# Kernel optimization log

Measured on AMD Instinct MI355X. Metric: run time of the kernel, lower is better.

The kernel has to match this reference:

```python
import jax, jax.numpy as jnp
import numpy as np

B, TQ, TKV, NPR, H, D = 4, 1024, 1024, 5, 16, 64
IN, OUT, R, P, NT = 1024, H * D, 64, 4096, 4
KV = NPR + TKV  # prompt tokens prepended to kv sequence


def setup_inputs() -> dict:
    key = jax.random.key(0)
    ks = jax.random.split(key, 20)
    n = lambda k, shp, s: jax.random.normal(k, shp, jnp.float32) * s
    W = 0.02  # weight init scale
    return {
        "pe": n(ks[0], (P, OUT), 1.0),
        "attn_output": n(ks[1], (B, TQ, OUT), 1.0),
        "q": n(ks[2], (B, H, TQ, D), 1.0),
        "kv_query": n(ks[3], (B, TKV, IN), 1.0),
        "attn_mask": jnp.zeros((TQ, KV), jnp.float32),
        "prompt": n(ks[4], (NT, NPR, IN), 1.0),
        "gates": n(ks[5], (1,), 1.0),
        "k_w1": n(ks[6], (IN, R), W), "k_w2": n(ks[7], (R, OUT), W),
        "v_w1": n(ks[8], (IN, R), W), "v_w2": n(ks[9], (R, OUT), W),
        "kp_w1": n(ks[10], (OUT, R), W), "kp_w2": n(ks[11], (R, OUT), W),
        "qp_w1": n(ks[12], (OUT, R), W), "qp_w2": n(ks[13], (R, OUT), W),
        "indices_a": jax.random.randint(ks[14], (B, TQ), 0, P),
        "indices_b": jax.random.randint(ks[15], (B, TKV), 0, P),
        "task_idx": jax.random.randint(ks[16], (B,), 0, NT),
    }


def reference(pe, attn_output, q, kv_query, attn_mask, prompt, gates,
              k_w1, k_w2, v_w1, v_w2, kp_w1, kp_w2, qp_w1, qp_w2,
              indices_a, indices_b, task_idx):
    # prompt selection + concat in front of kv sequence
    pr = prompt[task_idx]                                   # [B, NPR, IN]
    kv_x = jnp.concatenate([pr, kv_query], axis=1)          # [B, KV, IN]
    # positional features; key_pos is zero-padded over the prompt slots
    key_pos = jnp.pad(pe[indices_b], ((0, 0), (NPR, 0), (0, 0)))  # [B, KV, OUT]
    # low-rank projections
    k = (kv_x @ k_w1) @ k_w2 + (key_pos @ kp_w1) @ kp_w2    # [B, KV, OUT]
    v = (kv_x @ v_w1) @ v_w2                                # [B, KV, OUT]
    q_pos = (pe[indices_a] @ qp_w1) @ qp_w2                 # [B, TQ, OUT]
    qh = q + q_pos.reshape(B, TQ, H, D).transpose(0, 2, 1, 3)
    kh = k.reshape(B, KV, H, D).transpose(0, 2, 1, 3)
    vh = v.reshape(B, KV, H, D).transpose(0, 2, 1, 3)
    scores = jnp.einsum('bhqd,bhkd->bhqk', qh, kh) / np.float32(np.sqrt(D))
    scores = scores + attn_mask[None, None]                 # 2D mask path
    w = jax.nn.softmax(scores, axis=-1)                     # dropout = identity (eval)
    out = jnp.einsum('bhqk,bhkd->bhqd', w, vh)
    out = out.transpose(0, 2, 1, 3).reshape(B, TQ, OUT)
    return out * gates + attn_output
```

## Files before the change

kernel.cpp:

```cpp
#include <hip/hip_runtime.h>
#include <hip/hip_bf16.h>

#define B_    4
#define TQ_   1024
#define TKV_  1024
#define NPR_  5
#define H_    16
#define D_    64
#define IN_   1024
#define OUT_  1024
#define R_    64
#define P_    4096
#define KV_   1029
#define KVP_  1088
#define M1_   4116
#define M1P_  4160
#define MQ_   4096
#define NKT_  17
#define NQT_  16
#define MR_   (M1P_ * R_)
#define LOG2E_ 1.4426950408889634f
#define SQ_SCALE_ (0.125f * 1.4426950408889634f)

typedef __attribute__((ext_vector_type(8))) short short8;
typedef __attribute__((ext_vector_type(4))) float f32x4;
typedef __attribute__((ext_vector_type(4))) unsigned uint4v;
typedef __attribute__((ext_vector_type(2))) unsigned uint2v;

#define MFMA(a, b, c) __builtin_amdgcn_mfma_f32_16x16x32_bf16(a, b, c, 0, 0, 0)

#define AS1 __attribute__((address_space(1)))
#define AS3 __attribute__((address_space(3)))
#define GLDS(g, l) __builtin_amdgcn_global_load_lds((const AS1 void*)(g), (AS3 void*)(l), 16, 0, 0)

static __device__ __forceinline__ short f2bf(float f) {
  unsigned u = __builtin_bit_cast(unsigned, f);
  u += 0x7fffu + ((u >> 16) & 1u);
  return (short)(u >> 16);
}
static __device__ __forceinline__ float bf2f(unsigned short u) {
  return __builtin_bit_cast(float, (unsigned)u << 16);
}
static __device__ __forceinline__ short8 zero8() {
  short8 z = {0, 0, 0, 0, 0, 0, 0, 0};
  return z;
}
static __device__ __forceinline__ unsigned cvtpk(float lo, float hi) {
  unsigned r;
  asm("v_cvt_pk_bf16_f32 %0, %1, %2" : "=v"(r) : "v"(lo), "v"(hi));
  return r;
}
static __device__ __forceinline__ float vexp2(float x) {
  float r;
  asm("v_exp_f32 %0, %1" : "=v"(r) : "v"(x));
  return r;
}
static __device__ __forceinline__ void pl32(unsigned &a, unsigned &b) {
  asm("v_permlane32_swap_b32 %0, %1" : "+v"(a), "+v"(b));
}
static __device__ __forceinline__ void pl16(unsigned &a, unsigned &b) {
  asm("v_permlane16_swap_b32 %0, %1" : "+v"(a), "+v"(b));
}
static __device__ __forceinline__ float redsum4(float x) {
  unsigned a = __builtin_bit_cast(unsigned, x), b = a;
  pl16(a, b);
  x = __builtin_bit_cast(float, a) + __builtin_bit_cast(float, b);
  a = b = __builtin_bit_cast(unsigned, x);
  pl32(a, b);
  return __builtin_bit_cast(float, a) + __builtin_bit_cast(float, b);
}
static __device__ __forceinline__ void cd2bfrag(const f32x4 (&s)[4], short8 &p0, short8 &p1) {
  unsigned u00 = cvtpk(s[0][0], s[0][1]), u01 = cvtpk(s[0][2], s[0][3]);
  unsigned u10 = cvtpk(s[1][0], s[1][1]), u11 = cvtpk(s[1][2], s[1][3]);
  unsigned u20 = cvtpk(s[2][0], s[2][1]), u21 = cvtpk(s[2][2], s[2][3]);
  unsigned u30 = cvtpk(s[3][0], s[3][1]), u31 = cvtpk(s[3][2], s[3][3]);
  pl32(u00, u10); pl32(u01, u11); pl32(u20, u30); pl32(u21, u31);
  pl16(u00, u10); pl16(u01, u11); pl16(u20, u30); pl16(u21, u31);
  uint4v w0 = {u00, u01, u10, u11};
  uint4v w1 = {u20, u21, u30, u31};
  p0 = __builtin_bit_cast(short8, w0);
  p1 = __builtin_bit_cast(short8, w1);
}
static __device__ __forceinline__ short8 sum4pack(const unsigned short* p) {
  f32x4 lo = {0, 0, 0, 0}, hi = {0, 0, 0, 0};
#pragma unroll
  for (int c = 0; c < 4; ++c) {
    short8 v = *(const short8*)(p + (size_t)c * MR_);
#pragma unroll
    for (int j = 0; j < 4; ++j) {
      lo[j] += bf2f((unsigned short)v[j]);
      hi[j] += bf2f((unsigned short)v[j + 4]);
    }
  }
  uint4v u = {cvtpk(lo[0], lo[1]), cvtpk(lo[2], lo[3]),
              cvtpk(hi[0], hi[1]), cvtpk(hi[2], hi[3])};
  return __builtin_bit_cast(short8, u);
}

__global__ __launch_bounds__(256) void prep(
    const float* __restrict__ kw1, const float* __restrict__ vw1,
    const float* __restrict__ kpw1, const float* __restrict__ qpw1,
    const float* __restrict__ kw2, const float* __restrict__ vw2,
    const float* __restrict__ kpw2, const float* __restrict__ qpw2,
    const float* __restrict__ mask, const float* __restrict__ pe,
    short* __restrict__ w1t, short* __restrict__ w2t,
    short* __restrict__ pebf, int* __restrict__ mflags) {
  int bid = blockIdx.x;
  if (bid < 64) {
    int tid = bid * 256 + threadIdx.x;
    const float* w1s[4] = {kw1, vw1, kpw1, qpw1};
    const float* w2s[4] = {kw2, vw2, kpw2, qpw2};
    for (int i = tid; i < 4 * R_ * IN_; i += 64 * 256) {
      int m = i >> 16, p = i & 65535, r = p >> 10, k = p & 1023;
      w1t[i] = f2bf(w1s[m][k * R_ + r]);
    }
    for (int i = tid; i < 4 * OUT_ * R_; i += 64 * 256) {
      int m = i >> 16, p = i & 65535, o = p >> 6, r = p & 63;
      w2t[i] = f2bf(w2s[m][r * OUT_ + o]);
    }
  } else if (bid < 336) {
    int t = bid - 64;
    int qt = t / NKT_, kt = t % NKT_;
    int nz = 0;
    for (int it = 0; it < 16; ++it) {
      int e = it * 256 + threadIdx.x;
      int rr = e >> 6, cc = e & 63;
      int kv = kt * 64 + cc;
      if (kv < KV_) {
        float v = mask[(size_t)(qt * 64 + rr) * KV_ + kv];
        nz |= (v != 0.0f);
      }
    }
    __shared__ int snz[4];
    unsigned long long bv = __ballot(nz);
    if ((threadIdx.x & 63) == 0) snz[threadIdx.x >> 6] = (bv != 0ULL);
    __syncthreads();
    if (threadIdx.x == 0) mflags[t] = snz[0] | snz[1] | snz[2] | snz[3];
  } else {
    int pb = bid - 336;
#pragma unroll
    for (int it = 0; it < 8; ++it) {
      int i = pb * 16384 + it * 2048 + threadIdx.x * 8;
      f32x4 a0 = *(const f32x4*)(pe + i);
      f32x4 a1 = *(const f32x4*)(pe + i + 4);
      uint4v u = {cvtpk(a0[0], a0[1]), cvtpk(a0[2], a0[3]),
                  cvtpk(a1[0], a1[1]), cvtpk(a1[2], a1[3])};
      *(uint4v*)(pebf + i) = u;
    }
  }
}

__global__ __launch_bounds__(256) void stage1(
    const float* __restrict__ prompt, const float* __restrict__ kv_query,
    const short* __restrict__ pebf, const int* __restrict__ indices_a,
    const int* __restrict__ indices_b, const int* __restrict__ task_idx,
    const short* __restrict__ w1t, unsigned short* __restrict__ part) {
  int which = blockIdx.z;
  int chunk = blockIdx.y;
  int mbase = blockIdx.x * 64;
  int lane = threadIdx.x & 63, wave = threadIdx.x >> 6;
  int lrow = lane & 15, lg = lane >> 4;
  int row = mbase + wave * 16 + lrow;

  const float* asrc_f = nullptr;
  const short* asrc_b = nullptr;
  if (which == 0) {
    int r = min(row, M1_ - 1);
    int b = r / KV_, t = r - b * KV_;
    asrc_f = (t < NPR_) ? prompt + (size_t)(task_idx[b] * NPR_ + t) * IN_
                        : kv_query + (size_t)(b * TKV_ + t - NPR_) * IN_;
  } else if (which == 1) {
    int r = min(row, M1_ - 1);
    int b = r / KV_, t = r - b * KV_;
    if (t >= NPR_) asrc_b = pebf + (size_t)indices_b[b * TKV_ + t - NPR_] * OUT_;
  } else {
    int r = min(row, MQ_ - 1);
    asrc_b = pebf + (size_t)indices_a[r] * OUT_;
  }
  const short* bt0 = w1t + (size_t)((which == 0) ? 0 : (which == 1) ? 2 : 3) * (R_ * IN_);
  const short* bt1 = w1t + (size_t)1 * (R_ * IN_);
  int k0base = chunk * 256;

  const f32x4 fz = {0, 0, 0, 0};
  f32x4 acc0[4], acc1[4];
#pragma unroll
  for (int f = 0; f < 4; ++f) { acc0[f] = fz; acc1[f] = fz; }

#pragma unroll
  for (int ks = 0; ks < 8; ++ks) {
    int kc = k0base + ks * 32 + lg * 8;
    short8 bdat;
    if (which == 0) {
      f32x4 a0 = *(const f32x4*)(asrc_f + kc);
      f32x4 a1 = *(const f32x4*)(asrc_f + kc + 4);
      uint4v au = {cvtpk(a0[0], a0[1]), cvtpk(a0[2], a0[3]),
                   cvtpk(a1[0], a1[1]), cvtpk(a1[2], a1[3])};
      bdat = __builtin_bit_cast(short8, au);
    } else {
      bdat = asrc_b ? *(const short8*)(asrc_b + kc) : zero8();
    }
#pragma unroll
    for (int f = 0; f < 4; ++f) {
      short8 w0 = *(const short8*)(bt0 + (size_t)(f * 16 + lrow) * IN_ + kc);
      acc0[f] = MFMA(w0, bdat, acc0[f]);
      if (which == 0) {
        short8 w1f = *(const short8*)(bt1 + (size_t)(f * 16 + lrow) * IN_ + kc);
        acc1[f] = MFMA(w1f, bdat, acc1[f]);
      }
    }
  }
  int o0 = (which == 0) ? 0 : (which == 1) ? 2 : 3;
  size_t mrow = (size_t)(mbase + wave * 16 + lrow) * R_;
  unsigned short* p0 = part + (size_t)(o0 * 4 + chunk) * MR_ + mrow;
#pragma unroll
  for (int f = 0; f < 4; ++f) {
    uint2v w = {cvtpk(acc0[f][0], acc0[f][1]), cvtpk(acc0[f][2], acc0[f][3])};
    *(uint2v*)(p0 + f * 16 + lg * 4) = w;
  }
  if (which == 0) {
    unsigned short* p1 = part + (size_t)(4 + chunk) * MR_ + mrow;
#pragma unroll
    for (int f = 0; f < 4; ++f) {
      uint2v w = {cvtpk(acc1[f][0], acc1[f][1]), cvtpk(acc1[f][2], acc1[f][3])};
      *(uint2v*)(p1 + f * 16 + lg * 4) = w;
    }
  }
}

__global__ __launch_bounds__(256) void stage2(
    const unsigned short* __restrict__ part, const short* __restrict__ w2t,
    short* __restrict__ kbf, short* __restrict__ vtb, short* __restrict__ tqs) {
  int L = blockIdx.x;
  int lane = threadIdx.x & 63, wave = threadIdx.x >> 6;
  int lrow = lane & 15, lg = lane >> 4;
  const f32x4 fz = {0, 0, 0, 0};

  if (L < 272) {
    int virt = (L & 7) * 34 + (L >> 3);
    int mt = virt >> 2, nh = virt & 3;
    int orow = mt * 64 + wave * 16 + lrow;
    int ob = orow / KVP_, okv = orow - ob * KVP_;
    bool valid = (okv < KV_);
    int kt = okv >> 6, rin = okv & 63;
    int prow = ob * KV_ + min(okv, KV_ - 1);
    short8 b1[2], b2[2];
#pragma unroll
    for (int ks = 0; ks < 2; ++ks) {
      int kc = ks * 32 + lg * 8;
      b1[ks] = valid ? sum4pack(part + (size_t)prow * R_ + kc) : zero8();
      b2[ks] = valid ? sum4pack(part + (size_t)8 * MR_ + (size_t)prow * R_ + kc) : zero8();
    }
    const short* w2k  = w2t;
    const short* w2kp = w2t + (size_t)2 * (OUT_ * R_);
    int sw = (rin & 7) << 3;
#pragma unroll
    for (int i = 0; i < 4; ++i) {
      int nbase = (nh * 4 + i) * 64;
      int h = nbase >> 6;
      f32x4 acc[4];
#pragma unroll
      for (int f = 0; f < 4; ++f) acc[f] = fz;
#pragma unroll
      for (int ks = 0; ks < 2; ++ks) {
        int kc = ks * 32 + lg * 8;
#pragma unroll
        for (int f = 0; f < 4; ++f) {
          short8 aK  = *(const short8*)(w2k  + (size_t)(nbase + f * 16 + lrow) * R_ + kc);
          short8 aKP = *(const short8*)(w2kp + (size_t)(nbase + f * 16 + lrow) * R_ + kc);
          acc[f] = MFMA(aK,  b1[ks], acc[f]);
          acc[f] = MFMA(aKP, b2[ks], acc[f]);
        }
      }
      size_t tb = ((size_t)((ob * H_ + h) * NKT_ + kt) << 12);
#pragma unroll
      for (int f = 0; f < 4; ++f) {
        float v0 = valid ? acc[f][0] : 0.f, v1 = valid ? acc[f][1] : 0.f;
        float v2 = valid ? acc[f][2] : 0.f, v3 = valid ? acc[f][3] : 0.f;
        uint2v w = {cvtpk(v0, v1), cvtpk(v2, v3)};
        int d0 = f * 16 + lg * 4;
        *(uint2v*)(kbf + tb + rin * 64 + (d0 ^ sw)) = w;
      }
    }
  } else if (L < 544) {
    int Lm = L - 272;
    int virt = (Lm & 7) * 34 + (Lm >> 3);
    int cb = virt >> 2, oh = virt & 3;
    short8 afr[8];
#pragma unroll
    for (int f = 0; f < 4; ++f)
#pragma unroll
      for (int ks = 0; ks < 2; ++ks) {
        int crow = cb * 64 + f * 16 + lrow;
        int bb = crow / KVP_, kvr = crow - bb * KVP_;
        afr[f * 2 + ks] = (kvr < KV_)
            ? sum4pack(part + (size_t)4 * MR_ + (size_t)(bb * KV_ + kvr) * R_ + ks * 32 + lg * 8)
            : zero8();
      }
    int bb = (cb * 64) / KVP_;
    int kvbase = cb * 64 - bb * KVP_;
    int kt = kvbase >> 6;
    const short* w2v = w2t + (size_t)1 * (OUT_ * R_);
#pragma unroll
    for (int i = 0; i < 4; ++i) {
      int obase = (oh * 4 + i) * 64;
      int o = obase + wave * 16 + lrow;
      int h = o >> 6, d = o & 63;
      f32x4 acc[4];
#pragma unroll
      for (int f = 0; f < 4; ++f) acc[f] = fz;
#pragma unroll
      for (int ks = 0; ks < 2; ++ks) {
        short8 bw = *(const short8*)(w2v + (size_t)o * R_ + ks * 32 + lg * 8);
#pragma unroll
        for (int f = 0; f < 4; ++f) acc[f] = MFMA(afr[f * 2 + ks], bw, acc[f]);
      }
      int sw = (d & 7) << 3;
      size_t tb = ((size_t)((bb * H_ + h) * NKT_ + kt) << 12);
#pragma unroll
      for (int f = 0; f < 4; ++f) {
        int kvin0 = f * 16 + lg * 4;
        float v0 = (kvbase + kvin0 + 0 < KV_) ? acc[f][0] : 0.f;
        float v1 = (kvbase + kvin0 + 1 < KV_) ? acc[f][1] : 0.f;
        float v2 = (kvbase + kvin0 + 2 < KV_) ? acc[f][2] : 0.f;
        float v3 = (kvbase + kvin0 + 3 < KV_) ? acc[f][3] : 0.f;
        uint2v w = {cvtpk(v0, v1), cvtpk(v2, v3)};
        *(uint2v*)(vtb + tb + d * 64 + (kvin0 ^ sw)) = w;
      }
    }
  } else {
    int j = L - 544;
#pragma unroll
    for (int it = 0; it < 8; ++it) {
      int idx = j * 16384 + it * 2048 + threadIdx.x * 8;
      short8 v = sum4pack(part + (size_t)12 * MR_ + idx);
      *(short8*)(tqs + idx) = v;
    }
  }
}

__global__ __launch_bounds__(256, 4) void attn(
    const short* __restrict__ tqs, const short* __restrict__ w2t,
    const float* __restrict__ qin,
    const short* __restrict__ kbf, const short* __restrict__ vtb,
    const float* __restrict__ mask, const int* __restrict__ mflags,
    const float* __restrict__ gates, const float* __restrict__ attn_in,
    float* __restrict__ out) {
  int bid = blockIdx.x;
  int xcd = bid & 7, wg = bid >> 3;
  int qt = wg & 15, g = wg >> 4;
  int grp = xcd * 8 + g;
  int h = grp & 15, b = grp >> 4;

  int lane = threadIdx.x & 63, wave = threadIdx.x >> 6;
  int lrow = lane & 15, lg = lane >> 4;
  int qbase = qt * 64 + wave * 16;

  __shared__ __align__(16) short kvls[2][2][4096];

  const short* ktile = kbf + ((size_t)grp * NKT_ << 12);
  const short* vtile = vtb + ((size_t)grp * NKT_ << 12);
  const short* kg = ktile + wave * 512 + lane * 8;
  const short* vg = vtile + wave * 512 + lane * 8;

  int sw = (lrow & 7) << 3;
  int offA = (lg * 8) ^ sw;
  int offB = (32 + lg * 8) ^ sw;
  const short* p0A = &kvls[0][0][lrow * 64 + offA];
  const short* p0B = &kvls[0][0][lrow * 64 + offB];
  const short* p1A = &kvls[1][0][lrow * 64 + offA];
  const short* p1B = &kvls[1][0][lrow * 64 + offB];
  const int* mfp = mflags + qt * NKT_;

  auto stage = [&](int t, int bsel) {
    const short* ks = kg + ((size_t)t << 12);
    const short* vs = vg + ((size_t)t << 12);
    GLDS(ks,        &kvls[bsel][0][wave * 512]);
    GLDS(ks + 2048, &kvls[bsel][0][wave * 512 + 2048]);
    GLDS(vs,        &kvls[bsel][1][wave * 512]);
    GLDS(vs + 2048, &kvls[bsel][1][wave * 512 + 2048]);
  };

  stage(0, 0);

  const f32x4 fz = {0, 0, 0, 0};
  short8 qa0, qa1;
  {
    const short* w2q = w2t + (size_t)3 * (OUT_ * R_);
    f32x4 qs[4];
#pragma unroll
    for (int f = 0; f < 4; ++f) qs[f] = fz;
#pragma unroll
    for (int ks = 0; ks < 2; ++ks) {
      short8 tqf = *(const short8*)(tqs + (size_t)(b * TQ_ + qbase + lrow) * R_ + ks * 32 + lg * 8);
#pragma unroll
      for (int f = 0; f < 4; ++f) {
        short8 wf = *(const short8*)(w2q + (size_t)(h * 64 + f * 16 + lrow) * R_ + ks * 32 + lg * 8);
        qs[f] = MFMA(wf, tqf, qs[f]);
      }
    }
    const float* qrow = qin + (size_t)(b * TQ_ + qbase + lrow) * OUT_ + h * 64;
#pragma unroll
    for (int f = 0; f < 4; ++f) {
      f32x4 qv = *(const f32x4*)(qrow + f * 16 + lg * 4);
#pragma unroll
      for (int r = 0; r < 4; ++r) qs[f][r] = (qs[f][r] + qv[r]) * SQ_SCALE_;
    }
    cd2bfrag(qs, qa0, qa1);
  }

  f32x4 oacc[4];
#pragma unroll
  for (int f = 0; f < 4; ++f) oacc[f] = fz;
  float plsum = 0.f;

  asm volatile("s_waitcnt vmcnt(0)" ::: "memory");
  __builtin_amdgcn_sched_barrier(0);
  __builtin_amdgcn_s_barrier();
  __builtin_amdgcn_sched_barrier(0);

  auto tile = [&](int t, const short* pA, const short* pB, int nbsel, bool last) {
    if (!last) {
      stage(t + 1, nbsel);
      asm volatile("s_waitcnt vmcnt(4)" ::: "memory");
    } else {
      asm volatile("s_waitcnt vmcnt(0)" ::: "memory");
    }
    __builtin_amdgcn_sched_barrier(0);
    __builtin_amdgcn_s_barrier();
    __builtin_amdgcn_sched_barrier(0);

    f32x4 s[4];
#pragma unroll
    for (int f = 0; f < 4; ++f) {
      short8 kA = *(const short8*)(pA + f * 1024);
      short8 kB = *(const short8*)(pB + f * 1024);
      s[f] = MFMA(kA, qa0, fz);
      s[f] = MFMA(kB, qa1, s[f]);
    }
    short8 vfr[8];
#pragma unroll
    for (int f = 0; f < 4; ++f) {
      vfr[f * 2 + 0] = *(const short8*)(pA + 4096 + f * 1024);
      vfr[f * 2 + 1] = *(const short8*)(pB + 4096 + f * 1024);
    }
    if (mfp[t]) {
      int kvb = t * 64;
      const float* mrp = mask + (size_t)(qbase + lrow) * KV_;
#pragma unroll
      for (int f = 0; f < 4; ++f)
#pragma unroll
        for (int r = 0; r < 4; ++r) {
          int kv = kvb + f * 16 + lg * 4 + r;
          if (kv < KV_) s[f][r] += mrp[kv] * LOG2E_;
        }
    }
    if (last) {
#pragma unroll
      for (int f = 0; f < 4; ++f)
#pragma unroll
        for (int r = 0; r < 4; ++r) {
          int kv = t * 64 + f * 16 + lg * 4 + r;
          if (kv >= KV_) s[f][r] = -1e30f;
        }
    }
#pragma unroll
    for (int f = 0; f < 4; ++f)
#pragma unroll
      for (int r = 0; r < 4; ++r) s[f][r] = vexp2(s[f][r]);
    f32x4 st = (s[0] + s[1]) + (s[2] + s[3]);
    plsum += (st[0] + st[1]) + (st[2] + st[3]);
    short8 pb0, pb1;
    cd2bfrag(s, pb0, pb1);
#pragma unroll
    for (int f = 0; f < 4; ++f) {
      oacc[f] = MFMA(vfr[f * 2 + 0], pb0, oacc[f]);
      oacc[f] = MFMA(vfr[f * 2 + 1], pb1, oacc[f]);
    }
    __builtin_amdgcn_sched_barrier(0);
    __builtin_amdgcn_s_barrier();
    __builtin_amdgcn_sched_barrier(0);
  };

#pragma unroll 1
  for (int i = 0; i < 8; ++i) {
    tile(2 * i,     p0A, p0B, 1, false);
    tile(2 * i + 1, p1A, p1B, 0, false);
  }
  tile(16, p0A, p0B, 1, true);

  float lsum = redsum4(plsum);
  float sc = gates[0] / lsum;
  const float* ain = attn_in + (size_t)(b * TQ_ + qbase + lrow) * OUT_ + h * 64;
  float* op = out + (size_t)(b * TQ_ + qbase + lrow) * OUT_ + h * 64;
#pragma unroll
  for (int f = 0; f < 4; ++f) {
    f32x4 av = *(const f32x4*)(ain + f * 16 + lg * 4);
    f32x4 ov;
#pragma unroll
    for (int r = 0; r < 4; ++r) ov[r] = oacc[f][r] * sc + av[r];
    *(f32x4*)(op + f * 16 + lg * 4) = ov;
  }
}

extern "C" void kernel_launch(void* const* d_in, const int* in_sizes, int n_in,
                              void* d_out, int out_size, void* d_ws, size_t ws_size,
                              hipStream_t stream) {
  const float* pe          = (const float*)d_in[0];
  const float* attn_output = (const float*)d_in[1];
  const float* q           = (const float*)d_in[2];
  const float* kv_query    = (const float*)d_in[3];
  const float* attn_mask   = (const float*)d_in[4];
  const float* prompt      = (const float*)d_in[5];
  const float* gates       = (const float*)d_in[6];
  const float* k_w1        = (const float*)d_in[7];
  const float* k_w2        = (const float*)d_in[8];
  const float* v_w1        = (const float*)d_in[9];
  const float* v_w2        = (const float*)d_in[10];
  const float* kp_w1       = (const float*)d_in[11];
  const float* kp_w2       = (const float*)d_in[12];
  const float* qp_w1       = (const float*)d_in[13];
  const float* qp_w2       = (const float*)d_in[14];
  const int* indices_a     = (const int*)d_in[15];
  const int* indices_b     = (const int*)d_in[16];
  const int* task_idx      = (const int*)d_in[17];
  float* out = (float*)d_out;

  const size_t TILEB = (size_t)64 * NKT_ * 4096;

  short* ws   = (short*)d_ws;
  short* w1t  = ws;
  short* w2t  = w1t + 4 * 65536;
  unsigned short* part = (unsigned short*)(w2t + 4 * 65536);
  short* tqs  = (short*)(part + (size_t)16 * MR_);
  int* mflags = (int*)(tqs + (size_t)MQ_ * R_);
  short* pebf = (short*)mflags + 1024;
  short* kbf  = pebf;
  short* vtb  = kbf + TILEB;

  hipLaunchKernelGGL(prep, dim3(592), dim3(256), 0, stream,
                     k_w1, v_w1, kp_w1, qp_w1, k_w2, v_w2, kp_w2, qp_w2,
                     attn_mask, pe, w1t, w2t, pebf, mflags);
  hipLaunchKernelGGL(stage1, dim3(65, 4, 3), dim3(256), 0, stream,
                     prompt, kv_query, pebf, indices_a, indices_b, task_idx, w1t, part);
  hipLaunchKernelGGL(stage2, dim3(560), dim3(256), 0, stream,
                     part, w2t, kbf, vtb, tqs);
  hipLaunchKernelGGL(attn, dim3(1024), dim3(256), 0, stream,
                     tqs, w2t, q, kbf, vtb, attn_mask, mflags, gates, attn_output, out);
}
```

Before: 105.7 us.

## Fuse prep/stage1/stage2 into cooperative kernel and triple-buffer attention KV

```diff
diff --git a/kernel.cpp b/kernel.cpp
--- a/kernel.cpp
+++ b/kernel.cpp
@@ -1,5 +1,6 @@
 #include <hip/hip_runtime.h>
 #include <hip/hip_bf16.h>
+#include <hip/hip_cooperative_groups.h>
 
 #define B_    4
 #define TQ_   1024
@@ -10,7 +11,6 @@
 #define IN_   1024
 #define OUT_  1024
 #define R_    64
-#define P_    4096
 #define KV_   1029
 #define KVP_  1088
 #define M1_   4116
@@ -97,15 +97,27 @@
   return __builtin_bit_cast(short8, u);
 }
 
-__global__ __launch_bounds__(256) void prep(
+__global__ __launch_bounds__(256, 4) void proj(
+    const float* __restrict__ prompt, const float* __restrict__ kv_query,
+    const float* __restrict__ pe,
+    const int* __restrict__ indices_a, const int* __restrict__ indices_b,
+    const int* __restrict__ task_idx,
     const float* __restrict__ kw1, const float* __restrict__ vw1,
     const float* __restrict__ kpw1, const float* __restrict__ qpw1,
     const float* __restrict__ kw2, const float* __restrict__ vw2,
     const float* __restrict__ kpw2, const float* __restrict__ qpw2,
-    const float* __restrict__ mask, const float* __restrict__ pe,
+    const float* __restrict__ mask,
     short* __restrict__ w1t, short* __restrict__ w2t,
-    short* __restrict__ pebf, int* __restrict__ mflags) {
+    unsigned short* __restrict__ part,
+    short* __restrict__ kbf, short* __restrict__ vtb, short* __restrict__ tqs,
+    int* __restrict__ mflags) {
+  cooperative_groups::grid_group gg = cooperative_groups::this_grid();
   int bid = blockIdx.x;
+  int lane = threadIdx.x & 63, wave = threadIdx.x >> 6;
+  int lrow = lane & 15, lg = lane >> 4;
+  const f32x4 fz = {0, 0, 0, 0};
+  __shared__ int snz[4];
+
   if (bid < 64) {
     int tid = bid * 256 + threadIdx.x;
     const float* w1s[4] = {kw1, vw1, kpw1, qpw1};
@@ -131,110 +143,87 @@
         nz |= (v != 0.0f);
       }
     }
-    __shared__ int snz[4];
     unsigned long long bv = __ballot(nz);
     if ((threadIdx.x & 63) == 0) snz[threadIdx.x >> 6] = (bv != 0ULL);
     __syncthreads();
     if (threadIdx.x == 0) mflags[t] = snz[0] | snz[1] | snz[2] | snz[3];
-  } else {
-    int pb = bid - 336;
-#pragma unroll
-    for (int it = 0; it < 8; ++it) {
-      int i = pb * 16384 + it * 2048 + threadIdx.x * 8;
-      f32x4 a0 = *(const f32x4*)(pe + i);
-      f32x4 a1 = *(const f32x4*)(pe + i + 4);
-      uint4v u = {cvtpk(a0[0], a0[1]), cvtpk(a0[2], a0[3]),
-                  cvtpk(a1[0], a1[1]), cvtpk(a1[2], a1[3])};
-      *(uint4v*)(pebf + i) = u;
-    }
-  }
-}
-
-__global__ __launch_bounds__(256) void stage1(
-    const float* __restrict__ prompt, const float* __restrict__ kv_query,
-    const short* __restrict__ pebf, const int* __restrict__ indices_a,
-    const int* __restrict__ indices_b, const int* __restrict__ task_idx,
-    const short* __restrict__ w1t, unsigned short* __restrict__ part) {
-  int which = blockIdx.z;
-  int chunk = blockIdx.y;
-  int mbase = blockIdx.x * 64;
-  int lane = threadIdx.x & 63, wave = threadIdx.x >> 6;
-  int lrow = lane & 15, lg = lane >> 4;
-  int row = mbase + wave * 16 + lrow;
-
-  const float* asrc_f = nullptr;
-  const short* asrc_b = nullptr;
-  if (which == 0) {
-    int r = min(row, M1_ - 1);
-    int b = r / KV_, t = r - b * KV_;
-    asrc_f = (t < NPR_) ? prompt + (size_t)(task_idx[b] * NPR_ + t) * IN_
-                        : kv_query + (size_t)(b * TKV_ + t - NPR_) * IN_;
-  } else if (which == 1) {
-    int r = min(row, M1_ - 1);
-    int b = r / KV_, t = r - b * KV_;
-    if (t >= NPR_) asrc_b = pebf + (size_t)indices_b[b * TKV_ + t - NPR_] * OUT_;
-  } else {
-    int r = min(row, MQ_ - 1);
-    asrc_b = pebf + (size_t)indices_a[r] * OUT_;
-  }
-  const short* bt0 = w1t + (size_t)((which == 0) ? 0 : (which == 1) ? 2 : 3) * (R_ * IN_);
-  const short* bt1 = w1t + (size_t)1 * (R_ * IN_);
-  int k0base = chunk * 256;
-
-  const f32x4 fz = {0, 0, 0, 0};
-  f32x4 acc0[4], acc1[4];
-#pragma unroll
-  for (int f = 0; f < 4; ++f) { acc0[f] = fz; acc1[f] = fz; }
-
-#pragma unroll
-  for (int ks = 0; ks < 8; ++ks) {
-    int kc = k0base + ks * 32 + lg * 8;
-    short8 bdat;
-    if (which == 0) {
-      f32x4 a0 = *(const f32x4*)(asrc_f + kc);
-      f32x4 a1 = *(const f32x4*)(asrc_f + kc + 4);
-      uint4v au = {cvtpk(a0[0], a0[1]), cvtpk(a0[2], a0[3]),
-                   cvtpk(a1[0], a1[1]), cvtpk(a1[2], a1[3])};
-      bdat = __builtin_bit_cast(short8, au);
-    } else {
-      bdat = asrc_b ? *(const short8*)(asrc_b + kc) : zero8();
-    }
-#pragma unroll
-    for (int f = 0; f < 4; ++f) {
-      short8 w0 = *(const short8*)(bt0 + (size_t)(f * 16 + lrow) * IN_ + kc);
-      acc0[f] = MFMA(w0, bdat, acc0[f]);
+  }
+
+  gg.sync();
+
+  if (bid < 780) {
+    int which = bid / 260, rem = bid - which * 260;
+    int chunk = rem / 65, mt = rem - chunk * 65;
+    if (!(which == 2 && mt >= 64)) {
+      int mbase = mt * 64;
+      int row = mbase + wave * 16 + lrow;
+      const float* asrc = nullptr;
       if (which == 0) {
-        short8 w1f = *(const short8*)(bt1 + (size_t)(f * 16 + lrow) * IN_ + kc);
-        acc1[f] = MFMA(w1f, bdat, acc1[f]);
-      }
-    }
-  }
-  int o0 = (which == 0) ? 0 : (which == 1) ? 2 : 3;
-  size_t mrow = (size_t)(mbase + wave * 16 + lrow) * R_;
-  unsigned short* p0 = part + (size_t)(o0 * 4 + chunk) * MR_ + mrow;
-#pragma unroll
-  for (int f = 0; f < 4; ++f) {
-    uint2v w = {cvtpk(acc0[f][0], acc0[f][1]), cvtpk(acc0[f][2], acc0[f][3])};
-    *(uint2v*)(p0 + f * 16 + lg * 4) = w;
-  }
-  if (which == 0) {
-    unsigned short* p1 = part + (size_t)(4 + chunk) * MR_ + mrow;
-#pragma unroll
-    for (int f = 0; f < 4; ++f) {
-      uint2v w = {cvtpk(acc1[f][0], acc1[f][1]), cvtpk(acc1[f][2], acc1[f][3])};
-      *(uint2v*)(p1 + f * 16 + lg * 4) = w;
-    }
-  }
-}
-
-__global__ __launch_bounds__(256) void stage2(
-    const unsigned short* __restrict__ part, const short* __restrict__ w2t,
-    short* __restrict__ kbf, short* __restrict__ vtb, short* __restrict__ tqs) {
-  int L = blockIdx.x;
-  int lane = threadIdx.x & 63, wave = threadIdx.x >> 6;
-  int lrow = lane & 15, lg = lane >> 4;
-  const f32x4 fz = {0, 0, 0, 0};
-
+        int r = min(row, M1_ - 1);
+        int b = r / KV_, t = r - b * KV_;
+        asrc = (t < NPR_) ? prompt + (size_t)(task_idx[b] * NPR_ + t) * IN_
+                          : kv_query + (size_t)(b * TKV_ + t - NPR_) * IN_;
+      } else if (which == 1) {
+        int r = min(row, M1_ - 1);
+        int b = r / KV_, t = r - b * KV_;
+        if (t >= NPR_) asrc = pe + (size_t)indices_b[b * TKV_ + t - NPR_] * OUT_;
+      } else {
+        int r = min(row, MQ_ - 1);
+        asrc = pe + (size_t)indices_a[r] * OUT_;
+      }
+      const short* bt0 = w1t + (size_t)((which == 0) ? 0 : (which == 1) ? 2 : 3) * (R_ * IN_);
+      const short* bt1 = w1t + (size_t)1 * (R_ * IN_);
+      int k0base = chunk * 256;
+
+      f32x4 acc0[4], acc1[4];
+#pragma unroll
+      for (int f = 0; f < 4; ++f) { acc0[f] = fz; acc1[f] = fz; }
+
+#pragma unroll 2
+      for (int ks = 0; ks < 8; ++ks) {
+        int kc = k0base + ks * 32 + lg * 8;
+        short8 bdat;
+        if (asrc) {
+          f32x4 a0 = *(const f32x4*)(asrc + kc);
+          f32x4 a1 = *(const f32x4*)(asrc + kc + 4);
+          uint4v au = {cvtpk(a0[0], a0[1]), cvtpk(a0[2], a0[3]),
+                       cvtpk(a1[0], a1[1]), cvtpk(a1[2], a1[3])};
+          bdat = __builtin_bit_cast(short8, au);
+        } else {
+          bdat = zero8();
+        }
+#pragma unroll
+        for (int f = 0; f < 4; ++f) {
+          short8 w0 = *(const short8*)(bt0 + (size_t)(f * 16 + lrow) * IN_ + kc);
+          acc0[f] = MFMA(w0, bdat, acc0[f]);
+          if (which == 0) {
+            short8 w1f = *(const short8*)(bt1 + (size_t)(f * 16 + lrow) * IN_ + kc);
+            acc1[f] = MFMA(w1f, bdat, acc1[f]);
+          }
+        }
+      }
+      int o0 = (which == 0) ? 0 : (which == 1) ? 2 : 3;
+      size_t mrow = (size_t)(mbase + wave * 16 + lrow) * R_;
+      unsigned short* p0 = part + (size_t)(o0 * 4 + chunk) * MR_ + mrow;
+#pragma unroll
+      for (int f = 0; f < 4; ++f) {
+        uint2v w = {cvtpk(acc0[f][0], acc0[f][1]), cvtpk(acc0[f][2], acc0[f][3])};
+        *(uint2v*)(p0 + f * 16 + lg * 4) = w;
+      }
+      if (which == 0) {
+        unsigned short* p1 = part + (size_t)(4 + chunk) * MR_ + mrow;
+#pragma unroll
+        for (int f = 0; f < 4; ++f) {
+          uint2v w = {cvtpk(acc1[f][0], acc1[f][1]), cvtpk(acc1[f][2], acc1[f][3])};
+          *(uint2v*)(p1 + f * 16 + lg * 4) = w;
+        }
+      }
+    }
+  }
+
+  gg.sync();
+
+  int L = bid;
   if (L < 272) {
     int virt = (L & 7) * 34 + (L >> 3);
     int mt = virt >> 2, nh = virt & 3;
@@ -327,7 +316,7 @@
         *(uint2v*)(vtb + tb + d * 64 + (kvin0 ^ sw)) = w;
       }
     }
-  } else {
+  } else if (L < 560) {
     int j = L - 544;
 #pragma unroll
     for (int it = 0; it < 8; ++it) {
@@ -338,7 +327,7 @@
   }
 }
 
-__global__ __launch_bounds__(256, 4) void attn(
+__global__ __launch_bounds__(256, 3) void attn(
     const short* __restrict__ tqs, const short* __restrict__ w2t,
     const float* __restrict__ qin,
     const short* __restrict__ kbf, const short* __restrict__ vtb,
@@ -355,7 +344,7 @@
   int lrow = lane & 15, lg = lane >> 4;
   int qbase = qt * 64 + wave * 16;
 
-  __shared__ __align__(16) short kvls[2][2][4096];
+  __shared__ __align__(16) short kvls[3][2][4096];
 
   const short* ktile = kbf + ((size_t)grp * NKT_ << 12);
   const short* vtile = vtb + ((size_t)grp * NKT_ << 12);
@@ -369,6 +358,8 @@
   const short* p0B = &kvls[0][0][lrow * 64 + offB];
   const short* p1A = &kvls[1][0][lrow * 64 + offA];
   const short* p1B = &kvls[1][0][lrow * 64 + offB];
+  const short* p2A = &kvls[2][0][lrow * 64 + offA];
+  const short* p2B = &kvls[2][0][lrow * 64 + offB];
   const int* mfp = mflags + qt * NKT_;
 
   auto stage = [&](int t, int bsel) {
@@ -381,6 +372,12 @@
   };
 
   stage(0, 0);
+  stage(1, 1);
+
+  int fl = 0;
+#pragma unroll
+  for (int t = 0; t < NKT_; ++t) fl |= (mfp[t] ? 1 : 0) << t;
+  fl = __builtin_amdgcn_readfirstlane(fl);
 
   const f32x4 fz = {0, 0, 0, 0};
   short8 qa0, qa1;
@@ -413,21 +410,13 @@
   for (int f = 0; f < 4; ++f) oacc[f] = fz;
   float plsum = 0.f;
 
-  asm volatile("s_waitcnt vmcnt(0)" ::: "memory");
-  __builtin_amdgcn_sched_barrier(0);
-  __builtin_amdgcn_s_barrier();
-  __builtin_amdgcn_sched_barrier(0);
-
-  auto tile = [&](int t, const short* pA, const short* pB, int nbsel, bool last) {
-    if (!last) {
-      stage(t + 1, nbsel);
-      asm volatile("s_waitcnt vmcnt(4)" ::: "memory");
-    } else {
-      asm volatile("s_waitcnt vmcnt(0)" ::: "memory");
-    }
+  auto tile = [&](int t, const short* pA, const short* pB, int sb, int mode) {
+    if (mode == 2) asm volatile("s_waitcnt vmcnt(0)" ::: "memory");
+    else           asm volatile("s_waitcnt vmcnt(4)" ::: "memory");
     __builtin_amdgcn_sched_barrier(0);
     __builtin_amdgcn_s_barrier();
     __builtin_amdgcn_sched_barrier(0);
+    if (mode == 0) stage(t + 2, sb);
 
     f32x4 s[4];
 #pragma unroll
@@ -443,7 +432,7 @@
       vfr[f * 2 + 0] = *(const short8*)(pA + 4096 + f * 1024);
       vfr[f * 2 + 1] = *(const short8*)(pB + 4096 + f * 1024);
     }
-    if (mfp[t]) {
+    if ((fl >> t) & 1) {
       int kvb = t * 64;
       const float* mrp = mask + (size_t)(qbase + lrow) * KV_;
 #pragma unroll
@@ -454,7 +443,7 @@
           if (kv < KV_) s[f][r] += mrp[kv] * LOG2E_;
         }
     }
-    if (last) {
+    if (mode == 2) {
 #pragma unroll
       for (int f = 0; f < 4; ++f)
 #pragma unroll
@@ -476,17 +465,16 @@
       oacc[f] = MFMA(vfr[f * 2 + 0], pb0, oacc[f]);
       oacc[f] = MFMA(vfr[f * 2 + 1], pb1, oacc[f]);
     }
-    __builtin_amdgcn_sched_barrier(0);
-    __builtin_amdgcn_s_barrier();
-    __builtin_amdgcn_sched_barrier(0);
   };
 
 #pragma unroll 1
-  for (int i = 0; i < 8; ++i) {
-    tile(2 * i,     p0A, p0B, 1, false);
-    tile(2 * i + 1, p1A, p1B, 0, false);
-  }
-  tile(16, p0A, p0B, 1, true);
+  for (int i = 0; i < 5; ++i) {
+    tile(3 * i + 0, p0A, p0B, 2, 0);
+    tile(3 * i + 1, p1A, p1B, 0, 0);
+    tile(3 * i + 2, p2A, p2B, 1, 0);
+  }
+  tile(15, p0A, p0B, 2, 1);
+  tile(16, p1A, p1B, 0, 2);
 
   float lsum = redsum4(plsum);
   float sc = gates[0] / lsum;
@@ -532,18 +520,20 @@
   short* w2t  = w1t + 4 * 65536;
   unsigned short* part = (unsigned short*)(w2t + 4 * 65536);
   short* tqs  = (short*)(part + (size_t)16 * MR_);
-  int* mflags = (int*)(tqs + (size_t)MQ_ * R_);
-  short* pebf = (short*)mflags + 1024;
-  short* kbf  = pebf;
+  short* kbf  = tqs + (size_t)MQ_ * R_;
   short* vtb  = kbf + TILEB;
-
-  hipLaunchKernelGGL(prep, dim3(592), dim3(256), 0, stream,
-                     k_w1, v_w1, kp_w1, qp_w1, k_w2, v_w2, kp_w2, qp_w2,
-                     attn_mask, pe, w1t, w2t, pebf, mflags);
-  hipLaunchKernelGGL(stage1, dim3(65, 4, 3), dim3(256), 0, stream,
-                     prompt, kv_query, pebf, indices_a, indices_b, task_idx, w1t, part);
-  hipLaunchKernelGGL(stage2, dim3(560), dim3(256), 0, stream,
-                     part, w2t, kbf, vtb, tqs);
+  int* mflags = (int*)(vtb + TILEB);
+
+  void* args[] = {
+      (void*)&prompt, (void*)&kv_query, (void*)&pe,
+      (void*)&indices_a, (void*)&indices_b, (void*)&task_idx,
+      (void*)&k_w1, (void*)&v_w1, (void*)&kp_w1, (void*)&qp_w1,
+      (void*)&k_w2, (void*)&v_w2, (void*)&kp_w2, (void*)&qp_w2,
+      (void*)&attn_mask,
+      (void*)&w1t, (void*)&w2t, (void*)&part,
+      (void*)&kbf, (void*)&vtb, (void*)&tqs, (void*)&mflags};
+  hipLaunchCooperativeKernel(reinterpret_cast<void*>(proj), dim3(780), dim3(256),
+                             args, 0, stream);
   hipLaunchKernelGGL(attn, dim3(1024), dim3(256), 0, stream,
                      tqs, w2t, q, kbf, vtb, attn_mask, mflags, gates, attn_output, out);
 }
```

Measured after the change: 299.8 us. 184% more time.
